# Kernel optimization log

Hardware: AMD Instinct MI355X
Metric: run time of the kernel (lower is better)

## Reference

```python
import jax, jax.numpy as jnp
from jax import lax
import numpy as np

B, C, H, W, D = 4, 128, 32, 32, 32
NH = 4                 # num_heads (4*NH == 16 fc input channels)
DH = C // NH           # head dim = 32
N = H * W * D          # input_size = 32768
PROJ = 64              # proj_size
EPS = 1e-12


def setup_inputs() -> dict:
    key = jax.random.key(0)
    ks = jax.random.split(key, 12)
    s = 0.02
    return {
        "x": jax.random.normal(ks[0], (B, C, H, W, D), jnp.float32),
        "Wqkvv": jax.random.normal(ks[1], (4 * C, C), jnp.float32) * s,   # qkv_bias=False
        "W_fc": jax.random.normal(ks[2], (16, 4 * NH), jnp.float32) * s,  # Conv2d 1x1
        "b_fc": jnp.zeros((16,), jnp.float32),
        "W_dep": jax.random.normal(ks[3], (C, 16, 3, 3, 3), jnp.float32) * 0.05,  # groups=DH -> in/grp=16
        "b_dep": jnp.zeros((C,), jnp.float32),
        "W_E": jax.random.normal(ks[4], (PROJ, N), jnp.float32) * s,  # E = F (shared weights)
        "b_E": jnp.zeros((PROJ,), jnp.float32),
        "temperature": jnp.ones((NH, 1, 1), jnp.float32),
        "temperature2": jnp.ones((NH, 1, 1), jnp.float32),
        "rate": jnp.full((1,), 0.5, jnp.float32),
        "rate2": jnp.full((1,), 0.5, jnp.float32),
        "W_out": jax.random.normal(ks[5], (C // 2, C), jnp.float32) * s,
        "b_out": jnp.zeros((C // 2,), jnp.float32),
        "W_out2": jax.random.normal(ks[6], (C // 2, C), jnp.float32) * s,
        "b_out2": jnp.zeros((C // 2,), jnp.float32),
    }


def _l2norm(t):
    return t / jnp.maximum(jnp.linalg.norm(t, axis=-1, keepdims=True), EPS)


def reference(x, Wqkvv, W_fc, b_fc, W_dep, b_dep, W_E, b_E,
              temperature, temperature2, rate, rate2,
              W_out, b_out, W_out2, b_out2):
    Bc, Cc, Hc, Wc, Dc = x.shape
    Nc = Hc * Wc * Dc
    # tokens: [B, N, C]
    xf = jnp.transpose(x, (0, 2, 3, 4, 1)).reshape(Bc, Nc, Cc)
    qkvv = xf @ Wqkvv.T  # [B, N, 4C]

    # ---- fused grouped-conv branch ----
    f_all = jnp.transpose(qkvv.reshape(Bc, Nc, 4 * NH, DH), (0, 2, 1, 3))  # [B,16,N,DH]
    f = jnp.einsum('oi,bind->bond', W_fc, f_all) + b_fc[None, :, None, None]  # 1x1 conv
    f_conv = jnp.transpose(f, (0, 3, 1, 2)).reshape(Bc, 16 * DH, Hc, Wc, Dc)
    out_conv = lax.conv_general_dilated(
        f_conv, W_dep, window_strides=(1, 1, 1), padding='SAME',
        dimension_numbers=('NCDHW', 'OIDHW', 'NCDHW'), feature_group_count=DH)
    out_conv = out_conv + b_dep[None, :, None, None, None]
    out_conv = jnp.transpose(out_conv, (0, 2, 3, 4, 1)).reshape(Bc, Nc, Cc)

    # ---- dual attention ----
    qkvv5 = jnp.transpose(qkvv.reshape(Bc, Nc, 4, NH, DH), (2, 0, 3, 1, 4))  # [4,B,nh,N,dh]
    q = jnp.swapaxes(qkvv5[0], -2, -1)    # [B,nh,dh,N]
    k = jnp.swapaxes(qkvv5[1], -2, -1)
    v_CA = jnp.swapaxes(qkvv5[2], -2, -1)
    v_SA = jnp.swapaxes(qkvv5[3], -2, -1)

    k_proj = k @ W_E.T + b_E              # [B,nh,dh,proj]  (E)
    v_SA_proj = v_SA @ W_E.T + b_E        # shared weights   (F)

    qn = _l2norm(q)
    kn = _l2norm(k)

    # channel attention: [B,nh,dh,dh]
    attn_CA = jax.nn.softmax(jnp.einsum('bhdn,bhen->bhde', qn, kn) * temperature, axis=-1)
    x_CA = jnp.transpose(attn_CA @ v_CA, (0, 3, 1, 2)).reshape(Bc, Nc, Cc)  # [B,N,C]

    # spatial (Linformer-style) attention: [B,nh,N,proj]
    attn_SA = jax.nn.softmax(
        jnp.einsum('bhdn,bhdp->bhnp', qn, k_proj) * temperature2, axis=-1)
    x_SA = jnp.einsum('bhnp,bhdp->bhnd', attn_SA, v_SA_proj)  # [B,nh,N,dh]
    x_SA = jnp.transpose(x_SA, (0, 3, 1, 2)).reshape(Bc, Nc, Cc)  # faithful to torch permute

    x_SA = x_SA @ W_out.T + b_out    # [B,N,C/2]
    x_CA = x_CA @ W_out2.T + b_out2  # [B,N,C/2]
    x_attn = jnp.concatenate([x_SA, x_CA], axis=-1)
    return rate * x_attn + rate2 * out_conv
```

## Files before the change

### kernel.cpp

```cpp
#include <hip/hip_runtime.h>
#include <hip/hip_bf16.h>

typedef unsigned short u16;
typedef __attribute__((ext_vector_type(8))) short bf16x8;
typedef __attribute__((ext_vector_type(4))) float f32x4;

#define MFMA16(a,b,c) __builtin_amdgcn_mfma_f32_16x16x32_bf16((a),(b),(c),0,0,0)

__device__ __forceinline__ float bf2f(u16 u){ union{unsigned int i; float f;} v; v.i=((unsigned int)u)<<16; return v.f; }
__device__ __forceinline__ u16 f2bf(float f){ union{float f; unsigned int i;} v; v.f=f; unsigned int r=v.i+0x7fffu+((v.i>>16)&1u); return (u16)(r>>16); }
__device__ __forceinline__ unsigned int pk2(float a, float b){
  __hip_bfloat162 h = __float22bfloat162_rn(make_float2(a,b));
  union{ __hip_bfloat162 h; unsigned int u; } v; v.h = h; return v.u;
}

__global__ __launch_bounds__(256) void kcvt3(const float* __restrict__ WE, u16* __restrict__ WEb,
                                             const float* __restrict__ Wq, u16* __restrict__ Wqb,
                                             const float* __restrict__ Wo, u16* __restrict__ Wob){
  int bid = blockIdx.x;
  const float* src; u16* dst; int base;
  if(bid < 2048){ src = WE; dst = WEb; base = bid*1024; }
  else if(bid < 2112){ src = Wq; dst = Wqb; base = (bid-2048)*1024; }
  else { src = Wo; dst = Wob; base = (bid-2112)*1024; }
  int i = base + threadIdx.x*4;
  float4 v = *(const float4*)(src + i);
  ushort4 o; o.x = f2bf(v.x); o.y = f2bf(v.y); o.z = f2bf(v.z); o.w = f2bf(v.w);
  *(ushort4*)(dst + i) = o;
}

#define K1PAD 136
__global__ __launch_bounds__(256) void k1_qkvv(const float* __restrict__ x, const u16* __restrict__ Wqb, u16* __restrict__ qkvvT){
  __shared__ u16 lB[128*K1PAD];
  const int tile = blockIdx.x;
  const int b  = tile >> 8;
  const int n0 = (tile & 255) << 7;
  const int tid = threadIdx.x;
  const float* xb = x + (size_t)b*128*32768;
  {
    const int cb = (tid >> 4) << 1;
    const int m  = tid & 15;
    const int t8 = m << 3;
    const int swz = (m & 3) << 3;
    unsigned int* basep = (unsigned int*)lB;
    #pragma unroll
    for(int r=0;r<4;++r){
      const int c = cb + (r<<5);
      const float4* p0 = (const float4*)(xb + (size_t)c*32768 + n0 + t8);
      const float4* p1 = (const float4*)(xb + (size_t)(c+1)*32768 + n0 + t8);
      float4 a0 = p0[0], a1 = p0[1];
      float4 b0 = p1[0], b1 = p1[1];
      const int rot = (swz + c) & 127;
      int di = t8*68 + (rot>>1);
      basep[di      ] = pk2(a0.x, b0.x);
      basep[di+  68 ] = pk2(a0.y, b0.y);
      basep[di+ 136 ] = pk2(a0.z, b0.z);
      basep[di+ 204 ] = pk2(a0.w, b0.w);
      basep[di+ 272 ] = pk2(a1.x, b1.x);
      basep[di+ 340 ] = pk2(a1.y, b1.y);
      basep[di+ 408 ] = pk2(a1.z, b1.z);
      basep[di+ 476 ] = pk2(a1.w, b1.w);
    }
  }
  __syncthreads();
  const int wave = tid >> 6, lane = tid & 63;
  const int wm = (wave & 1) << 6;
  const int wn = (wave >> 1) << 6;
  const int lm = lane & 15, lq = lane >> 4;
  u16* outb = qkvvT + (size_t)b*512*32768;
  for(int s=0;s<4;++s){
    const int oc0 = s << 7;
    f32x4 acc[4][4] = {};
    const u16* Arow = Wqb + (oc0 + wm + lm)*128 + lq*8;
    #pragma unroll
    for(int ks=0; ks<4; ++ks){
      bf16x8 af[4], bfr[4];
      #pragma unroll
      for(int mt=0;mt<4;++mt) af[mt] = *(const bf16x8*)(Arow + mt*2048 + ks*32);
      #pragma unroll
      for(int nt=0;nt<4;++nt){
        const int tr = wn + nt*16 + lm;
        const int rot = ((((tr>>3)&3)<<3) + ks*32 + lq*8) & 127;
        bfr[nt] = *(const bf16x8*)(&lB[tr*K1PAD + rot]);
      }
      #pragma unroll
      for(int mt=0;mt<4;++mt)
        #pragma unroll
        for(int nt=0;nt<4;++nt)
          acc[mt][nt] = MFMA16(af[mt], bfr[nt], acc[mt][nt]);
    }
    #pragma unroll
    for(int mt=0;mt<4;++mt){
      const int ocr = oc0 + wm + mt*16 + lq*4;
      #pragma unroll
      for(int nt=0;nt<4;++nt){
        const int n = n0 + wn + nt*16 + lm;
        #pragma unroll
        for(int r=0;r<4;++r) outb[(size_t)(ocr+r)*32768 + n] = f2bf(acc[mt][nt][r]);
      }
    }
  }
}

__global__ void k2_weff(const float* __restrict__ Wdep, const float* __restrict__ Wfc,
                        const float* __restrict__ bdep, const float* __restrict__ bfc,
                        float* __restrict__ W_eff, float* __restrict__ bias_eff){
  int idx = blockIdx.x*256 + threadIdx.x;
  if(idx < 55296){
    int ol = idx & 3;
    int k  = (idx >> 2) % 27;
    int j  = (idx / 108) & 15;
    int g  = idx / 1728;
    int oc = g*4 + ol;
    float s = 0.f;
    for(int o=0;o<16;++o) s += Wdep[(oc*16 + o)*27 + k] * Wfc[o*16 + j];
    W_eff[idx] = s;
  }
  if(idx < 128){
    float s = bdep[idx];
    for(int o=0;o<16;++o){
      float wsum = 0.f;
      for(int k=0;k<27;++k) wsum += Wdep[(idx*16 + o)*27 + k];
      s += wsum * bfc[o];
    }
    bias_eff[idx] = s;
  }
}

__global__ __launch_bounds__(256) void k2b_norms(const u16* __restrict__ qkvvT, float* __restrict__ invn){
  const int b = blockIdx.x >> 8, c = blockIdx.x & 255;
  const u16* row = qkvvT + ((size_t)b*512 + c)*32768;
  float s = 0.f;
  for(int n = threadIdx.x*8; n < 32768; n += 2048){
    bf16x8 v = *(const bf16x8*)(row + n);
    #pragma unroll
    for(int j=0;j<8;++j){ float f = bf2f((u16)v[j]); s += f*f; }
  }
  for(int off=32; off; off>>=1) s += __shfl_down(s, off, 64);
  __shared__ float wsum[4];
  if((threadIdx.x & 63)==0) wsum[threadIdx.x>>6] = s;
  __syncthreads();
  if(threadIdx.x==0){
    float t = wsum[0]+wsum[1]+wsum[2]+wsum[3];
    invn[blockIdx.x] = 1.0f / fmaxf(sqrtf(t), 1e-12f);
  }
}

__global__ __launch_bounds__(256) void k3_proj(const u16* __restrict__ qkvvT, const u16* __restrict__ WEb,
                                               float* __restrict__ kp, float* __restrict__ vp){
  const int kc = blockIdx.x;
  const int b  = blockIdx.y;
  const int ts = blockIdx.z >> 1;
  const int rh = (blockIdx.z & 1) << 6;
  const int wave = threadIdx.x >> 6, lane = threadIdx.x & 63;
  const int lm = lane & 15, lq = lane >> 4;
  const int coff = ts ? 384 : 128;
  const u16* Arow = qkvvT + ((size_t)b*512 + coff + rh + wave*16 + lm)*32768 + kc*1024 + lq*8;
  f32x4 acc[4] = {};
  for(int ks=0; ks<32; ++ks){
    bf16x8 af = *(const bf16x8*)(Arow + ks*32);
    #pragma unroll
    for(int nt=0;nt<4;++nt){
      bf16x8 bfr = *(const bf16x8*)(WEb + (size_t)(nt*16 + lm)*32768 + kc*1024 + ks*32 + lq*8);
      acc[nt] = MFMA16(af, bfr, acc[nt]);
    }
  }
  float* out = (ts ? vp : kp) + (size_t)b*128*64;
  const int r0 = rh + wave*16 + lq*4;
  #pragma unroll
  for(int nt=0;nt<4;++nt){
    const int p = nt*16 + lm;
    #pragma unroll
    for(int r=0;r<4;++r) atomicAdd(&out[(r0+r)*64 + p], acc[nt][r]);
  }
}

__global__ __launch_bounds__(64) void k4_gram(const u16* __restrict__ qkvvT, float* __restrict__ G){
  const int kc = blockIdx.x, b = blockIdx.y, h = blockIdx.z;
  const int lane = threadIdx.x, lm = lane & 15, lq = lane >> 4;
  const u16* qb = qkvvT + ((size_t)b*512 + h*32)*32768 + kc*512 + lq*8;
  const u16* kb = qb + (size_t)128*32768;
  f32x4 acc[2][2] = {};
  for(int ks=0; ks<16; ++ks){
    bf16x8 af[2], bfr[2];
    af[0]  = *(const bf16x8*)(qb + (size_t)lm*32768 + ks*32);
    af[1]  = *(const bf16x8*)(qb + (size_t)(16+lm)*32768 + ks*32);
    bfr[0] = *(const bf16x8*)(kb + (size_t)lm*32768 + ks*32);
    bfr[1] = *(const bf16x8*)(kb + (size_t)(16+lm)*32768 + ks*32);
    #pragma unroll
    for(int mt=0;mt<2;++mt)
      #pragma unroll
      for(int nt=0;nt<2;++nt) acc[mt][nt] = MFMA16(af[mt], bfr[nt], acc[mt][nt]);
  }
  float* Gb = G + (size_t)(b*4 + h)*1024;
  #pragma unroll
  for(int mt=0;mt<2;++mt)
    #pragma unroll
    for(int nt=0;nt<2;++nt)
      #pragma unroll
      for(int r=0;r<4;++r){
        int d = mt*16 + lq*4 + r, e = nt*16 + lm;
        atomicAdd(&Gb[d*32 + e], acc[mt][nt][r]);
      }
}

__global__ __launch_bounds__(256) void k4b_softmax_m2(const float* __restrict__ G, const float* __restrict__ invn,
                                                      const float* __restrict__ temp, const float* __restrict__ Wout2,
                                                      u16* __restrict__ M2){
  const int b = blockIdx.x >> 2, h = blockIdx.x & 3;
  __shared__ float A[32][33];
  const float* Gb = G + (size_t)(b*4 + h)*1024;
  const float* inb = invn + b*256;
  const float th = temp[h];
  const int tid = threadIdx.x;
  if(tid < 32){
    const int d = tid;
    const float iq = inb[h*32 + d];
    float row[32]; float mx = -1e30f;
    #pragma unroll
    for(int e=0;e<32;++e){
      float v = Gb[d*32+e] * iq * inb[128 + h*32 + e] * th;
      row[e] = v; mx = fmaxf(mx, v);
    }
    float s = 0.f;
    #pragma unroll
    for(int e=0;e<32;++e){ float ee = __expf(row[e]-mx); row[e] = ee; s += ee; }
    const float rs = 1.0f/s;
    #pragma unroll
    for(int e=0;e<32;++e) A[d][e] = row[e]*rs;
  }
  __syncthreads();
  for(int o = tid; o < 2048; o += 256){
    const int j = o >> 5, e = o & 31;
    float s = 0.f;
    #pragma unroll
    for(int d=0;d<32;++d) s += Wout2[j*128 + h*32 + d] * A[d][e];
    M2[((size_t)b*64 + j)*128 + h*32 + e] = f2bf(s);
  }
}

__global__ __launch_bounds__(256) void k5_xsa(const u16* __restrict__ qkvvT, const float* __restrict__ kp,
                                              const float* __restrict__ vp, const float* __restrict__ invn,
                                              const float* __restrict__ bE, const float* __restrict__ temp2,
                                              u16* __restrict__ xsa){
  const int b = blockIdx.z, h = blockIdx.y, n0 = blockIdx.x*256;
  __shared__ float lkp[32][64], lvp[32][64], liq[32];
  const int tid = threadIdx.x;
  for(int o = tid; o < 2048; o += 256){
    int d = o >> 6, p = o & 63;
    float be = bE[p];
    size_t base = ((size_t)b*128 + h*32 + d)*64 + p;
    lkp[d][p] = kp[base] + be;
    lvp[d][p] = vp[base] + be;
  }
  if(tid < 32) liq[tid] = invn[b*256 + h*32 + tid];
  __syncthreads();
  const int n = n0 + tid;
  const u16* qb = qkvvT + ((size_t)b*512 + h*32)*32768 + n;
  const float t2 = temp2[h];
  float s[64];
  #pragma unroll
  for(int p=0;p<64;++p) s[p]=0.f;
  for(int d=0; d<32; ++d){
    float qv = bf2f(qb[(size_t)d*32768]) * liq[d];
    #pragma unroll
    for(int p=0;p<64;++p) s[p] += qv * lkp[d][p];
  }
  float mx = -1e30f;
  #pragma unroll
  for(int p=0;p<64;++p){ s[p] *= t2; mx = fmaxf(mx, s[p]); }
  float sum = 0.f;
  #pragma unroll
  for(int p=0;p<64;++p){ s[p] = __expf(s[p]-mx); sum += s[p]; }
  const float r = 1.0f/sum;
  u16* ob = xsa + (((size_t)b*4 + h)*32)*32768 + n;
  for(int d=0; d<32; ++d){
    float acc = 0.f;
    #pragma unroll
    for(int p=0;p<64;++p) acc += s[p]*lvp[d][p];
    ob[(size_t)d*32768] = f2bf(acc*r);
  }
}

#define CSX 36
#define CSZ 360
__global__ __launch_bounds__(256,4) void kconv(const u16* __restrict__ qkvvT, const float* __restrict__ W_eff,
                                               const float* __restrict__ bias_eff, u16* __restrict__ convo){
  __shared__ float lf[18*CSZ];
  const int zt = blockIdx.x >> 2, yt = blockIdx.x & 3;
  const int g = blockIdx.y, b = blockIdx.z;
  const int tid = threadIdx.x;
  const int z0 = zt << 4, y0 = yt << 3;
  const int lz = (tid >> 5) << 1;
  const int vy = (tid >> 2) & 7;
  const int x0 = (tid & 3) << 3;
  float acc[2][4][8];
  #pragma unroll
  for(int o=0;o<2;++o)
    #pragma unroll
    for(int oc=0;oc<4;++oc)
      #pragma unroll
      for(int xi=0;xi<8;++xi) acc[o][oc][xi] = 0.f;
  const u16* qb = qkvvT + (size_t)b*512*32768;
  const int sz = tid / 10, sy = tid - sz*10;
  const int gz = z0 + sz - 1, gy = y0 + sy - 1;
  const bool srow_ok = (tid < 180) && ((unsigned)gz < 32u) && ((unsigned)gy < 32u);
  float2* d2 = (float2*)&lf[sz*CSZ + sy*CSX];
  const float* Wgbase = W_eff + (size_t)(g*16)*108;

  for(int p=0;p<16;++p){
    __syncthreads();
    if(tid < 180){
      if(srow_ok){
        const u16* src = qb + ((size_t)(p*32 + g))*32768 + gz*1024 + gy*32;
        float carry = 0.f;
        #pragma unroll
        for(int q=0;q<4;++q){
          bf16x8 v = *(const bf16x8*)(src + q*8);
          float w0=bf2f((u16)v[0]), w1=bf2f((u16)v[1]), w2=bf2f((u16)v[2]), w3=bf2f((u16)v[3]);
          float w4=bf2f((u16)v[4]), w5=bf2f((u16)v[5]), w6=bf2f((u16)v[6]), w7=bf2f((u16)v[7]);
          d2[q*4+0] = make_float2(carry, w0);
          d2[q*4+1] = make_float2(w1, w2);
          d2[q*4+2] = make_float2(w3, w4);
          d2[q*4+3] = make_float2(w5, w6);
          carry = w7;
        }
        d2[16] = make_float2(carry, 0.f);
      } else {
        #pragma unroll
        for(int i=0;i<17;++i) d2[i] = make_float2(0.f, 0.f);
      }
    }
    __syncthreads();
    const float* Wg = Wgbase + p*108;
    #pragma unroll
    for(int dy=0;dy<3;++dy){
      #pragma unroll
      for(int dz=0;dz<4;++dz){
        const float* row = &lf[(lz+dz)*CSZ + (vy+dy)*CSX + x0];
        float4 fa = *(const float4*)(row);
        float4 fb = *(const float4*)(row+4);
        float2 fc = *(const float2*)(row+8);
        float fw[10] = {fa.x,fa.y,fa.z,fa.w, fb.x,fb.y,fb.z,fb.w, fc.x,fc.y};
        if(dz < 3){
          const float* Wb = Wg + (dz*3+dy)*12;
          #pragma unroll
          for(int kx=0;kx<3;++kx){
            float4 wv = *(const float4*)(Wb + kx*4);
            #pragma unroll
            for(int xi=0;xi<8;++xi){
              float f = fw[xi+kx];
              acc[0][0][xi] += wv.x*f; acc[0][1][xi] += wv.y*f;
              acc[0][2][xi] += wv.z*f; acc[0][3][xi] += wv.w*f;
            }
          }
        }
        if(dz > 0){
          const float* Wb = Wg + ((dz-1)*3+dy)*12;
          #pragma unroll
          for(int kx=0;kx<3;++kx){
            float4 wv = *(const float4*)(Wb + kx*4);
            #pragma unroll
            for(int xi=0;xi<8;++xi){
              float f = fw[xi+kx];
              acc[1][0][xi] += wv.x*f; acc[1][1][xi] += wv.y*f;
              acc[1][2][xi] += wv.z*f; acc[1][3][xi] += wv.w*f;
            }
          }
        }
      }
    }
  }
  const float4 bi = *(const float4*)(bias_eff + g*4);
  #pragma unroll
  for(int o=0;o<2;++o){
    const int nb = (z0 + lz + o)*1024 + (y0+vy)*32 + x0;
    u16* ob = convo + ((size_t)b*32768 + nb)*128 + g*4;
    #pragma unroll
    for(int xi=0;xi<8;++xi){
      unsigned long long pk = (unsigned long long)f2bf(acc[o][0][xi] + bi.x)
                            | ((unsigned long long)f2bf(acc[o][1][xi] + bi.y) << 16)
                            | ((unsigned long long)f2bf(acc[o][2][xi] + bi.z) << 32)
                            | ((unsigned long long)f2bf(acc[o][3][xi] + bi.w) << 48);
      *(unsigned long long*)(ob + (size_t)xi*128) = pk;
    }
  }
}

#define K6PAD 136
__global__ __launch_bounds__(256) void k6_out(const u16* __restrict__ qkvvT, const u16* __restrict__ xsa,
                                              const u16* __restrict__ conv, const u16* __restrict__ M2,
                                              const u16* __restrict__ Woutb, const float* __restrict__ bout,
                                              const float* __restrict__ bout2, const float* __restrict__ rate,
                                              const float* __restrict__ rate2, float* __restrict__ out){
  __shared__ u16 lA[128*K6PAD];
  const int tile = blockIdx.x;
  const int b  = tile >> 8;
  const int n0 = (tile & 255) << 7;
  const int tid = threadIdx.x;
  const int hh = (n0 >> 8) & 3;
  const int dh = n0 >> 10;
  const u16* xseg = xsa + (((size_t)b*4 + hh)*32 + dh)*32768 + ((size_t)(n0 & 255) << 7);
  {
    const int r = tid >> 1, off = (tid & 1) << 6;
    const u16* src = xseg + r*128 + off;
    u16* dst = &lA[r*K6PAD + off];
    #pragma unroll
    for(int q=0;q<8;++q) *(bf16x8*)(dst + q*8) = *(const bf16x8*)(src + q*8);
  }
  __syncthreads();
  const int wave = tid >> 6, lane = tid & 63;
  const int lm = lane & 15, lq = lane >> 4;
  f32x4 accS[2][4] = {};
  #pragma unroll
  for(int ks=0;ks<4;++ks){
    bf16x8 a0 = *(const bf16x8*)(&lA[(wave*32 + lm)*K6PAD + ks*32 + lq*8]);
    bf16x8 a1 = *(const bf16x8*)(&lA[(wave*32 + 16 + lm)*K6PAD + ks*32 + lq*8]);
    #pragma unroll
    for(int nt=0;nt<4;++nt){
      bf16x8 bw = *(const bf16x8*)(Woutb + (nt*16 + lm)*128 + ks*32 + lq*8);
      accS[0][nt] = MFMA16(a0, bw, accS[0][nt]);
      accS[1][nt] = MFMA16(a1, bw, accS[1][nt]);
    }
  }
  __syncthreads();
  {
    const int cb = tid >> 4, t8 = (tid & 15) << 3;
    const u16* vb = qkvvT + ((size_t)b*512 + 256)*32768 + n0;
    #pragma unroll
    for(int r2=0;r2<8;++r2){
      int c = cb + (r2<<4);
      bf16x8 v = *(const bf16x8*)(vb + (size_t)c*32768 + t8);
      #pragma unroll
      for(int j=0;j<8;++j) lA[(t8+j)*K6PAD + c] = (u16)v[j];
    }
  }
  __syncthreads();
  f32x4 accC[2][4] = {};
  #pragma unroll
  for(int ks=0;ks<4;++ks){
    bf16x8 a0 = *(const bf16x8*)(&lA[(wave*32 + lm)*K6PAD + ks*32 + lq*8]);
    bf16x8 a1 = *(const bf16x8*)(&lA[(wave*32 + 16 + lm)*K6PAD + ks*32 + lq*8]);
    #pragma unroll
    for(int nt=0;nt<4;++nt){
      bf16x8 bm = *(const bf16x8*)(M2 + ((size_t)b*64 + nt*16 + lm)*128 + ks*32 + lq*8);
      accC[0][nt] = MFMA16(a0, bm, accC[0][nt]);
      accC[1][nt] = MFMA16(a1, bm, accC[1][nt]);
    }
  }
  const float rt = rate[0], rt2 = rate2[0];
  float* ob = out + ((size_t)b*32768 + n0)*128;
  const u16* cbp = conv + ((size_t)b*32768 + n0)*128;
  #pragma unroll
  for(int mt=0;mt<2;++mt){
    #pragma unroll
    for(int r=0;r<4;++r){
      const int tok = wave*32 + mt*16 + lq*4 + r;
      #pragma unroll
      for(int nt=0;nt<4;++nt){
        const int j = nt*16 + lm;
        float sa = accS[mt][nt][r] + bout[j];
        float ca = accC[mt][nt][r] + bout2[j];
        float c1 = bf2f(cbp[(size_t)tok*128 + j]);
        float c2 = bf2f(cbp[(size_t)tok*128 + 64 + j]);
        ob[(size_t)tok*128 + j]      = rt*sa + rt2*c1;
        ob[(size_t)tok*128 + 64 + j] = rt*ca + rt2*c2;
      }
    }
  }
}

extern "C" void kernel_launch(void* const* d_in, const int* in_sizes, int n_in,
                              void* d_out, int out_size, void* d_ws, size_t ws_size,
                              hipStream_t stream){
  const float* x     = (const float*)d_in[0];
  const float* Wq    = (const float*)d_in[1];
  const float* Wfc   = (const float*)d_in[2];
  const float* bfc   = (const float*)d_in[3];
  const float* Wdep  = (const float*)d_in[4];
  const float* bdep  = (const float*)d_in[5];
  const float* WE    = (const float*)d_in[6];
  const float* bE    = (const float*)d_in[7];
  const float* temp  = (const float*)d_in[8];
  const float* temp2 = (const float*)d_in[9];
  const float* rate  = (const float*)d_in[10];
  const float* rate2 = (const float*)d_in[11];
  const float* Wout  = (const float*)d_in[12];
  const float* bout  = (const float*)d_in[13];
  const float* Wout2 = (const float*)d_in[14];
  const float* bout2 = (const float*)d_in[15];
  float* outp = (float*)d_out;

  char* w = (char*)d_ws;
  size_t off = 0;
  auto alloc = [&](size_t bytes)->char*{ char* p = w + off; off += (bytes + 255) & ~(size_t)255; return p; };
  u16*   qkvvT  = (u16*)  alloc((size_t)4*512*32768*2);
  u16*   xsa    = (u16*)  alloc((size_t)4*4*32*32768*2);
  u16*   convb  = (u16*)  alloc((size_t)4*32768*128*2);
  float* W_eff  = (float*)alloc(55296*4);
  float* biasef = (float*)alloc(128*4);
  float* invn   = (float*)alloc(1024*4);
  float* kp     = (float*)alloc(32768*4);
  float* vp     = (float*)alloc(32768*4);
  float* G      = (float*)alloc(16384*4);
  u16*   M2     = (u16*)  alloc(32768*2);
  u16*   WEb    = (u16*)  alloc((size_t)2097152*2);
  u16*   Wqb    = (u16*)  alloc(65536*2);
  u16*   Woutb  = (u16*)  alloc(8192*2);

  hipMemsetAsync(kp, 0, (size_t)(32768+32768+16384)*4, stream);

  kcvt3         <<<2120,          256, 0, stream>>>(WE, WEb, Wq, Wqb, Wout, Woutb);
  k1_qkvv       <<<1024,          256, 0, stream>>>(x, Wqb, qkvvT);
  k2_weff       <<<216,           256, 0, stream>>>(Wdep, Wfc, bdep, bfc, W_eff, biasef);
  k2b_norms     <<<1024,          256, 0, stream>>>(qkvvT, invn);
  k3_proj       <<<dim3(32,4,4),  256, 0, stream>>>(qkvvT, WEb, kp, vp);
  k4_gram       <<<dim3(64,4,4),   64, 0, stream>>>(qkvvT, G);
  k4b_softmax_m2<<<16,            256, 0, stream>>>(G, invn, temp, Wout2, M2);
  k5_xsa        <<<dim3(128,4,4), 256, 0, stream>>>(qkvvT, kp, vp, invn, bE, temp2, xsa);
  kconv         <<<dim3(8,32,4),  256, 0, stream>>>(qkvvT, W_eff, biasef, convb);
  k6_out        <<<1024,          256, 0, stream>>>(qkvvT, xsa, convb, M2, Woutb, bout, bout2, rate, rate2, outp);
}
```

Baseline: 636.8 us.

## Double-buffer conv input tiles to overlap global loads with compute

The depthwise conv kernel now keeps two LDS buffers. It prefetches the next input-channel slab into registers while computing on the current one, then writes it to the alternate buffer, which leaves one barrier per iteration instead of two. This is meant to hide global memory latency behind the FMA work. In exchange it doubles LDS use and lowers the occupancy hint from 4 to 3 blocks per CU. It also holds the prefetch registers live during compute.

```diff
diff --git a/kernel.cpp b/kernel.cpp
--- a/kernel.cpp
+++ b/kernel.cpp
@@ -283,9 +283,10 @@
 
 #define CSX 36
 #define CSZ 360
-__global__ __launch_bounds__(256,4) void kconv(const u16* __restrict__ qkvvT, const float* __restrict__ W_eff,
+#define CBUF 6480
+__global__ __launch_bounds__(256,3) void kconv(const u16* __restrict__ qkvvT, const float* __restrict__ W_eff,
                                                const float* __restrict__ bias_eff, u16* __restrict__ convo){
-  __shared__ float lf[18*CSZ];
+  __shared__ float lf[2*CBUF];
   const int zt = blockIdx.x >> 2, yt = blockIdx.x & 3;
   const int g = blockIdx.y, b = blockIdx.z;
   const int tid = threadIdx.x;
@@ -304,39 +305,50 @@
   const int sz = tid / 10, sy = tid - sz*10;
   const int gz = z0 + sz - 1, gy = y0 + sy - 1;
   const bool srow_ok = (tid < 180) && ((unsigned)gz < 32u) && ((unsigned)gy < 32u);
-  float2* d2 = (float2*)&lf[sz*CSZ + sy*CSX];
   const float* Wgbase = W_eff + (size_t)(g*16)*108;
 
+  if(tid < 180 && !srow_ok){
+    float2* a0 = (float2*)&lf[sz*CSZ + sy*CSX];
+    float2* a1 = (float2*)&lf[CBUF + sz*CSZ + sy*CSX];
+    #pragma unroll
+    for(int i=0;i<17;++i){ a0[i] = make_float2(0.f,0.f); a1[i] = make_float2(0.f,0.f); }
+  }
+  if(srow_ok){
+    const u16* src = qb + ((size_t)g)*32768 + gz*1024 + gy*32;
+    bf16x8 pre[4];
+    #pragma unroll
+    for(int q=0;q<4;++q) pre[q] = *(const bf16x8*)(src + q*8);
+    float2* d2 = (float2*)&lf[sz*CSZ + sy*CSX];
+    float carry = 0.f;
+    #pragma unroll
+    for(int q=0;q<4;++q){
+      bf16x8 v = pre[q];
+      float w0=bf2f((u16)v[0]), w1=bf2f((u16)v[1]), w2=bf2f((u16)v[2]), w3=bf2f((u16)v[3]);
+      float w4=bf2f((u16)v[4]), w5=bf2f((u16)v[5]), w6=bf2f((u16)v[6]), w7=bf2f((u16)v[7]);
+      d2[q*4+0] = make_float2(carry, w0);
+      d2[q*4+1] = make_float2(w1, w2);
+      d2[q*4+2] = make_float2(w3, w4);
+      d2[q*4+3] = make_float2(w5, w6);
+      carry = w7;
+    }
+    d2[16] = make_float2(carry, 0.f);
+  }
+  __syncthreads();
+
   for(int p=0;p<16;++p){
-    __syncthreads();
-    if(tid < 180){
-      if(srow_ok){
-        const u16* src = qb + ((size_t)(p*32 + g))*32768 + gz*1024 + gy*32;
-        float carry = 0.f;
-        #pragma unroll
-        for(int q=0;q<4;++q){
-          bf16x8 v = *(const bf16x8*)(src + q*8);
-          float w0=bf2f((u16)v[0]), w1=bf2f((u16)v[1]), w2=bf2f((u16)v[2]), w3=bf2f((u16)v[3]);
-          float w4=bf2f((u16)v[4]), w5=bf2f((u16)v[5]), w6=bf2f((u16)v[6]), w7=bf2f((u16)v[7]);
-          d2[q*4+0] = make_float2(carry, w0);
-          d2[q*4+1] = make_float2(w1, w2);
-          d2[q*4+2] = make_float2(w3, w4);
-          d2[q*4+3] = make_float2(w5, w6);
-          carry = w7;
-        }
-        d2[16] = make_float2(carry, 0.f);
-      } else {
-        #pragma unroll
-        for(int i=0;i<17;++i) d2[i] = make_float2(0.f, 0.f);
-      }
-    }
-    __syncthreads();
+    const float* lfb = lf + (p&1)*CBUF;
+    bf16x8 nxt[4];
+    if(p < 15 && srow_ok){
+      const u16* src = qb + ((size_t)((p+1)*32 + g))*32768 + gz*1024 + gy*32;
+      #pragma unroll
+      for(int q=0;q<4;++q) nxt[q] = *(const bf16x8*)(src + q*8);
+    }
     const float* Wg = Wgbase + p*108;
     #pragma unroll
     for(int dy=0;dy<3;++dy){
       #pragma unroll
       for(int dz=0;dz<4;++dz){
-        const float* row = &lf[(lz+dz)*CSZ + (vy+dy)*CSX + x0];
+        const float* row = &lfb[(lz+dz)*CSZ + (vy+dy)*CSX + x0];
         float4 fa = *(const float4*)(row);
         float4 fb = *(const float4*)(row+4);
         float2 fc = *(const float2*)(row+8);
@@ -369,6 +381,23 @@
         }
       }
     }
+    if(p < 15 && srow_ok){
+      float2* d2 = (float2*)&lf[((p+1)&1)*CBUF + sz*CSZ + sy*CSX];
+      float carry = 0.f;
+      #pragma unroll
+      for(int q=0;q<4;++q){
+        bf16x8 v = nxt[q];
+        float w0=bf2f((u16)v[0]), w1=bf2f((u16)v[1]), w2=bf2f((u16)v[2]), w3=bf2f((u16)v[3]);
+        float w4=bf2f((u16)v[4]), w5=bf2f((u16)v[5]), w6=bf2f((u16)v[6]), w7=bf2f((u16)v[7]);
+        d2[q*4+0] = make_float2(carry, w0);
+        d2[q*4+1] = make_float2(w1, w2);
+        d2[q*4+2] = make_float2(w3, w4);
+        d2[q*4+3] = make_float2(w5, w6);
+        carry = w7;
+      }
+      d2[16] = make_float2(carry, 0.f);
+    }
+    __syncthreads();
   }
   const float4 bi = *(const float4*)(bias_eff + g*4);
   #pragma unroll
```

Measured after the change: 857.4 us. +34.6%, slower.

## Double-buffer conv halo tiles in bf16 LDS via direct global-to-LDS loads

Applied to the files above, without the earlier changes.

The depthwise conv kernel now stages input halo tiles as raw bf16 in two LDS buffers, filled with global_load_lds DMA instead of register loads that convert to float, and uses an XOR swizzled column layout. Loading the next channel slice overlaps with computing the current one, and bf16-to-float unpacking moves into the compute loop. This halves the LDS footprint and removes the per-slice load-convert-store stall, at the cost of extra unpack ALU work, edge handling logic, and reliance on the asynchronous LDS load ordering being correct around the barriers.

```diff
diff --git a/kernel.cpp b/kernel.cpp
--- a/kernel.cpp
+++ b/kernel.cpp
@@ -12,6 +12,10 @@
 __device__ __forceinline__ unsigned int pk2(float a, float b){
   __hip_bfloat162 h = __float22bfloat162_rn(make_float2(a,b));
   union{ __hip_bfloat162 h; unsigned int u; } v; v.h = h; return v.u;
+}
+__device__ __forceinline__ void gload16(const void* g, void* l){
+  __builtin_amdgcn_global_load_lds((const __attribute__((address_space(1))) unsigned int*)g,
+                                   (__attribute__((address_space(3))) unsigned int*)l, 16, 0, 0);
 }
 
 __global__ __launch_bounds__(256) void kcvt3(const float* __restrict__ WE, u16* __restrict__ WEb,
@@ -281,11 +285,11 @@
   }
 }
 
-#define CSX 36
-#define CSZ 360
+#define KCH 5760
 __global__ __launch_bounds__(256,4) void kconv(const u16* __restrict__ qkvvT, const float* __restrict__ W_eff,
                                                const float* __restrict__ bias_eff, u16* __restrict__ convo){
-  __shared__ float lf[18*CSZ];
+  __shared__ __align__(16) u16 lfA[KCH];
+  __shared__ __align__(16) u16 lfB[KCH];
   const int zt = blockIdx.x >> 2, yt = blockIdx.x & 3;
   const int g = blockIdx.y, b = blockIdx.z;
   const int tid = threadIdx.x;
@@ -293,54 +297,58 @@
   const int lz = (tid >> 5) << 1;
   const int vy = (tid >> 2) & 7;
   const int x0 = (tid & 3) << 3;
-  float acc[2][4][8];
-  #pragma unroll
-  for(int o=0;o<2;++o)
-    #pragma unroll
-    for(int oc=0;oc<4;++oc)
-      #pragma unroll
-      for(int xi=0;xi<8;++xi) acc[o][oc][xi] = 0.f;
-  const u16* qb = qkvvT + (size_t)b*512*32768;
-  const int sz = tid / 10, sy = tid - sz*10;
-  const int gz = z0 + sz - 1, gy = y0 + sy - 1;
-  const bool srow_ok = (tid < 180) && ((unsigned)gz < 32u) && ((unsigned)gy < 32u);
-  float2* d2 = (float2*)&lf[sz*CSZ + sy*CSX];
-  const float* Wgbase = W_eff + (size_t)(g*16)*108;
-
-  for(int p=0;p<16;++p){
-    __syncthreads();
-    if(tid < 180){
-      if(srow_ok){
-        const u16* src = qb + ((size_t)(p*32 + g))*32768 + gz*1024 + gy*32;
-        float carry = 0.f;
-        #pragma unroll
-        for(int q=0;q<4;++q){
-          bf16x8 v = *(const bf16x8*)(src + q*8);
-          float w0=bf2f((u16)v[0]), w1=bf2f((u16)v[1]), w2=bf2f((u16)v[2]), w3=bf2f((u16)v[3]);
-          float w4=bf2f((u16)v[4]), w5=bf2f((u16)v[5]), w6=bf2f((u16)v[6]), w7=bf2f((u16)v[7]);
-          d2[q*4+0] = make_float2(carry, w0);
-          d2[q*4+1] = make_float2(w1, w2);
-          d2[q*4+2] = make_float2(w3, w4);
-          d2[q*4+3] = make_float2(w5, w6);
-          carry = w7;
-        }
-        d2[16] = make_float2(carry, 0.f);
-      } else {
-        #pragma unroll
-        for(int i=0;i<17;++i) d2[i] = make_float2(0.f, 0.f);
-      }
-    }
-    __syncthreads();
-    const float* Wg = Wgbase + p*108;
+  const int wave = tid >> 6;
+  const u16* qb = qkvvT + (size_t)b*512*32768 + (size_t)g*32768;
+
+  int goff[3]; bool vld[3];
+  u16 *lbA[3], *lbB[3];
+  #pragma unroll
+  for(int i=0;i<3;++i){
+    const int ob = i*4096 + tid*16;
+    const int s  = ob >> 6;
+    const int cph= (ob >> 4) & 3;
+    const int szv= s/10, syv = s - szv*10;
+    const int r  = (syv>>1)&3;
+    const int cl = cph ^ r;
+    const int gz = z0 + szv - 1, gy = y0 + syv - 1;
+    vld[i] = (ob < 11520) && ((unsigned)gz < 32u) && ((unsigned)gy < 32u);
+    goff[i] = gz*1024 + gy*32 + cl*8;
+    const int wb = (i*4096 + wave*1024) >> 1;
+    lbA[i] = lfA + wb; lbB[i] = lfB + wb;
+  }
+
+  float acc[2][4][8] = {};
+
+  {
+    bf16x8 z8 = {};
+    for(int o = tid*8; o < KCH; o += 2048){ *(bf16x8*)(lfA+o) = z8; *(bf16x8*)(lfB+o) = z8; }
+  }
+  __syncthreads();
+  #pragma unroll
+  for(int i=0;i<3;++i) if(vld[i]) gload16(qb + goff[i], lbA[i]);
+  __syncthreads();
+
+  auto COMPUTE = [&](const u16* __restrict__ lb, const float* __restrict__ Wg){
     #pragma unroll
     for(int dy=0;dy<3;++dy){
       #pragma unroll
       for(int dz=0;dz<4;++dz){
-        const float* row = &lf[(lz+dz)*CSZ + (vy+dy)*CSX + x0];
-        float4 fa = *(const float4*)(row);
-        float4 fb = *(const float4*)(row+4);
-        float2 fc = *(const float2*)(row+8);
-        float fw[10] = {fa.x,fa.y,fa.z,fa.w, fb.x,fb.y,fb.z,fb.w, fc.x,fc.y};
+        const int syp = vy + dy;
+        const u16* row = lb + (((lz+dz)*10 + syp) << 5);
+        const int r = (syp>>1)&3;
+        const int mc  = (x0>>3) ^ r;
+        const int lcc = (x0 ? (x0>>3)-1 : 0) ^ r;
+        const int rcc = (x0<24 ? (x0>>3)+1 : 3) ^ r;
+        uint4 mv = *(const uint4*)(row + (mc<<3));
+        unsigned int ldw = *(const unsigned int*)(row + (lcc<<3) + 6);
+        unsigned int rdw = *(const unsigned int*)(row + (rcc<<3));
+        float fw[10];
+        fw[0] = x0 ? __uint_as_float(ldw & 0xffff0000u) : 0.f;
+        fw[1] = __uint_as_float(mv.x<<16); fw[2] = __uint_as_float(mv.x & 0xffff0000u);
+        fw[3] = __uint_as_float(mv.y<<16); fw[4] = __uint_as_float(mv.y & 0xffff0000u);
+        fw[5] = __uint_as_float(mv.z<<16); fw[6] = __uint_as_float(mv.z & 0xffff0000u);
+        fw[7] = __uint_as_float(mv.w<<16); fw[8] = __uint_as_float(mv.w & 0xffff0000u);
+        fw[9] = (x0<24) ? __uint_as_float(rdw<<16) : 0.f;
         if(dz < 3){
           const float* Wb = Wg + (dz*3+dy)*12;
           #pragma unroll
@@ -369,7 +377,26 @@
         }
       }
     }
-  }
+  };
+
+  const float* Wgbase = W_eff + (size_t)(g*16)*108;
+  for(int p2=0;p2<16;p2+=2){
+    {
+      const u16* src = qb + (size_t)(p2+1)*32*32768;
+      #pragma unroll
+      for(int i=0;i<3;++i) if(vld[i]) gload16(src + goff[i], lbB[i]);
+    }
+    COMPUTE(lfA, Wgbase + p2*108);
+    __syncthreads();
+    if(p2+2 < 16){
+      const u16* src = qb + (size_t)(p2+2)*32*32768;
+      #pragma unroll
+      for(int i=0;i<3;++i) if(vld[i]) gload16(src + goff[i], lbA[i]);
+    }
+    COMPUTE(lfB, Wgbase + (p2+1)*108);
+    __syncthreads();
+  }
+
   const float4 bi = *(const float4*)(bias_eff + g*4);
   #pragma unroll
   for(int o=0;o<2;++o){
```

Result: slower. 899.8 us (+41.3%).
